# Optimization experiments

Measured on AMD Instinct MI355X. Metric: run time of the kernel, lower is better.

## Reference

```python
import math
import jax, jax.numpy as jnp
from jax import lax
import numpy as np

DIM = 1024
SEED = 2024
N_STEPS = math.ceil(math.log2(DIM) * 0.3) * DIM  # 3072, the KacLayer default


def _make_walk(seed):
    """Seed-derived schedule of Kac random-walk rotations: pairs (i,j), i!=j, and angles."""
    rng = np.random.default_rng(seed)
    ii = rng.integers(0, DIM, N_STEPS).astype(np.int32)
    jj = ((ii + rng.integers(1, DIM, N_STEPS)) % DIM).astype(np.int32)  # guaranteed j != i
    th = rng.uniform(0.0, 2.0 * np.pi, N_STEPS)
    return (jnp.asarray(ii), jnp.asarray(jj),
            jnp.asarray(np.cos(th), dtype=jnp.float32),
            jnp.asarray(np.sin(th), dtype=jnp.float32))

_WALK1 = _make_walk(SEED * 2)      # kac_random_walk_(x, seed*2, n_steps)
_WALK2 = _make_walk(SEED * 2 + 1)  # kac_random_walk_(x, seed*2+1, n_steps)


def _kac_walk(x, walk):
    """Apply N_STEPS sequential 2-coordinate Givens rotations to rows of x [T, DIM]."""
    ii, jj, cs, sn = walk
    def step(x, a):
        i, j, c, s = a
        xi = x[:, i]
        xj = x[:, j]
        x = x.at[:, i].set(c * xi - s * xj)
        x = x.at[:, j].set(s * xi + c * xj)
        return x, None
    x, _ = lax.scan(step, x, (ii, jj, cs, sn))
    return x


def setup_inputs() -> dict:
    key = jax.random.key(0)
    kx, kw, kb, kv = jax.random.split(key, 4)
    x = jax.random.normal(kx, (8, 4096, DIM), dtype=jnp.float32)
    W = jax.random.normal(kw, (DIM, DIM), dtype=jnp.float32) * (1.0 / math.sqrt(DIM))
    b = jax.random.normal(kb, (DIM,), dtype=jnp.float32)
    vec = jax.random.normal(kv, (DIM,), dtype=jnp.float32) * (1.0 / math.sqrt(DIM))
    return {"x": x, "W": W, "b": b, "vec": vec}


def reference(x, W, b, vec):
    # frozen inner layer: y = layer(x)
    y = jnp.einsum("bsd,ed->bse", x, W) + b
    # adapter path on flattened tokens
    x2 = x.reshape(-1, DIM)          # x.view(-1, dim)
    yp = _kac_walk(x2, _WALK1)       # kac_random_walk_(x2, seed*2, n_steps)
    yp = vec * yp                    # elementwise scale by learned vector
    yp = _kac_walk(yp, _WALK2)       # kac_random_walk_(yp, seed*2+1, n_steps)
    return y + yp.reshape(y.shape)
```

## Files before the change

### kernel.cpp

```cpp
#include <hip/hip_runtime.h>


#define NSTEPS 3072
#define NCHUNK 26
#define NRAW (256 * NCHUNK)
#define MAXS 4608
#define MAXLEV 256

typedef __attribute__((ext_vector_type(8))) short short8;
typedef __attribute__((ext_vector_type(4))) float f32x4;

struct U128 { unsigned long long lo, hi; };

__device__ __forceinline__ U128 mul128(U128 a, U128 b) {
  U128 r;
  r.lo = a.lo * b.lo;
  r.hi = __umul64hi(a.lo, b.lo) + a.lo * b.hi + a.hi * b.lo;
  return r;
}
__device__ __forceinline__ U128 add128(U128 a, U128 b) {
  U128 r; r.lo = a.lo + b.lo;
  r.hi = a.hi + b.hi + ((r.lo < a.lo) ? 1ull : 0ull);
  return r;
}
__device__ __forceinline__ U128 pcg_mult() {
  return U128{4865540595714422341ull, 2549297995355413924ull};
}
__device__ __forceinline__ U128 pcg_step(U128 st, U128 inc) {
  return add128(mul128(st, pcg_mult()), inc);
}
__device__ __forceinline__ unsigned long long pcg_out(U128 st) {
  unsigned long long x = st.hi ^ st.lo;
  unsigned int rot = (unsigned int)(st.hi >> 58);
  return (x >> rot) | (x << ((64u - rot) & 63u));
}

__device__ void pcg_seed(unsigned int seedval, U128* st, U128* inc) {
  unsigned int pool[4];
  unsigned int hc = 0x43b0d7e5u;
  auto hashmix = [&hc](unsigned int v) {
    v ^= hc; hc *= 0x931e8875u; v *= hc; v ^= v >> 16; return v;
  };
  auto mixf = [](unsigned int x, unsigned int y) {
    unsigned int r = x * 0xca01f9ddu - y * 0x4973f715u;
    r ^= r >> 16; return r;
  };
  pool[0] = hashmix(seedval);
  pool[1] = hashmix(0u); pool[2] = hashmix(0u); pool[3] = hashmix(0u);
  for (int s = 0; s < 4; ++s)
    for (int d = 0; d < 4; ++d)
      if (s != d) pool[d] = mixf(pool[d], hashmix(pool[s]));
  unsigned int gc = 0x8b51f9ddu;
  unsigned int wv[8];
  for (int k = 0; k < 8; ++k) {
    unsigned int dv = pool[k & 3];
    dv ^= gc; gc *= 0x58f38dedu; dv *= gc; dv ^= dv >> 16;
    wv[k] = dv;
  }
  unsigned long long o0 = (unsigned long long)wv[0] | ((unsigned long long)wv[1] << 32);
  unsigned long long o1 = (unsigned long long)wv[2] | ((unsigned long long)wv[3] << 32);
  unsigned long long o2 = (unsigned long long)wv[4] | ((unsigned long long)wv[5] << 32);
  unsigned long long o3 = (unsigned long long)wv[6] | ((unsigned long long)wv[7] << 32);
  U128 initstate = { o1, o0 };
  U128 initseq   = { o3, o2 };
  U128 icc; icc.lo = (initseq.lo << 1) | 1ull;
  icc.hi = (initseq.hi << 1) | (initseq.lo >> 63);
  *inc = icc;
  U128 s0 = {0ull, 0ull};
  s0 = pcg_step(s0, icc);
  s0 = add128(s0, initstate);
  s0 = pcg_step(s0, icc);
  *st = s0;
}

__device__ U128 pcg_advance(U128 st, U128 inc, unsigned long long delta) {
  U128 am = {1ull, 0ull}, ap = {0ull, 0ull};
  U128 cm = pcg_mult(), cp = inc;
  while (delta) {
    if (delta & 1ull) {
      am = mul128(am, cm);
      ap = add128(mul128(ap, cm), cp);
    }
    cp = mul128(add128(cm, U128{1ull, 0ull}), cp);
    cm = mul128(cm, cm);
    delta >>= 1;
  }
  return add128(mul128(st, am), ap);
}

__device__ __forceinline__ double first_draw(unsigned int seed) {
  U128 st, inc;
  pcg_seed(seed, &st, &inc);
  st = pcg_step(st, inc);
  return (double)(pcg_out(st) >> 11) * (1.0 / 9007199254740992.0);
}

__device__ __forceinline__ unsigned short f32_to_bf16(float f) {
  unsigned int u = __builtin_bit_cast(unsigned int, f);
  unsigned int r = u + 0x7fffu + ((u >> 16) & 1u);
  return (unsigned short)(r >> 16);
}

__global__ __launch_bounds__(256) void gen_sched_kernel(uint4* __restrict__ ps0,
                                                        uint4* __restrict__ ps1,
                                                        int* __restrict__ hdr,
                                                        float* __restrict__ diag) {
  __shared__ unsigned long long raw[NRAW];
  __shared__ unsigned int s_ij[NSTEPS];
  __shared__ unsigned short s_list[2 * NSTEPS];
  __shared__ short s_predA[NSTEPS];
  __shared__ short s_predB[NSTEPS];
  __shared__ unsigned short s_lev[NSTEPS];
  __shared__ int s_cnt[1024];
  __shared__ int s_base[1025];
  __shared__ int s_lcnt[MAXLEV];
  __shared__ int s_lbase[MAXLEV];
  __shared__ int s_rej, s_p64, s_changed, s_maxlev, s_ns;
  const int w = blockIdx.x;
  const int t = threadIdx.x;

  if (w == 0 && t == 0) {
    int m1 = first_draw(42u)    != 0.7739560485559633;
    int m2 = first_draw(0u)     != 0.6369616873214543;
    int m3 = first_draw(12345u) != 0.22733602246716966;
    if (m1 + m2 + m3 >= 2)
      diag[0] = 3.0e8f + (float)(m1 + 2 * m2 + 4 * m3) * 3.0e7f;
  }

  U128 st, inc;
  pcg_seed(4048u + (unsigned int)w, &st, &inc);
  U128 mine = pcg_advance(st, inc, (unsigned long long)t * NCHUNK);
  for (int q = 0; q < NCHUNK; ++q) {
    mine = pcg_step(mine, inc);
    raw[t * NCHUNK + q] = pcg_out(mine);
  }
  if (t == 0) { s_rej = 0; s_maxlev = 1; }
  __syncthreads();

  auto u32at = [&](int m) -> unsigned int {
    unsigned long long v = raw[m >> 1];
    return (m & 1) ? (unsigned int)(v >> 32) : (unsigned int)v;
  };

  for (int k = t; k < NSTEPS; k += 256) {
    unsigned long long m = (unsigned long long)u32at(NSTEPS + k) * 1023ull;
    if ((unsigned int)m < 4u) atomicAdd(&s_rej, 1);
  }
  __syncthreads();

  if (s_rej == 0) {
    for (int k = t; k < NSTEPS; k += 256) {
      unsigned int iv = u32at(k) >> 22;
      unsigned long long m = (unsigned long long)u32at(NSTEPS + k) * 1023ull;
      unsigned int off = 1u + (unsigned int)(m >> 32);
      unsigned int jv = (iv + off) & 1023u;
      s_ij[k] = (iv << 16) | jv;
    }
    if (t == 0) s_p64 = NSTEPS;
  } else if (t == 0) {
    int p = 0;
    for (int k = 0; k < NSTEPS; ++k) s_ij[k] = (u32at(p++) >> 22) << 16;
    for (int k = 0; k < NSTEPS; ++k) {
      unsigned long long m = (unsigned long long)u32at(p++) * 1023ull;
      unsigned int lo = (unsigned int)m;
      if (lo < 1023u) {
        while (lo < 4u) { m = (unsigned long long)u32at(p++) * 1023ull; lo = (unsigned int)m; }
      }
      unsigned int off = 1u + (unsigned int)(m >> 32);
      unsigned int iv = s_ij[k] >> 16;
      s_ij[k] = (iv << 16) | ((iv + off) & 1023u);
    }
    s_p64 = (p + 1) >> 1;
  }
  __syncthreads();

  for (int c = t; c < 1024; c += 256) s_cnt[c] = 0;
  __syncthreads();
  for (int k = t; k < NSTEPS; k += 256) {
    atomicAdd(&s_cnt[s_ij[k] >> 16], 1);
    atomicAdd(&s_cnt[s_ij[k] & 0xffffu], 1);
  }
  __syncthreads();
  if (t < 64) {
    int loc[16], tot = 0;
    #pragma unroll
    for (int q = 0; q < 16; ++q) { loc[q] = s_cnt[t * 16 + q]; tot += loc[q]; }
    int sc = tot;
    for (int off = 1; off < 64; off <<= 1) {
      int v = __shfl_up(sc, off);
      if (t >= off) sc += v;
    }
    int base = sc - tot;
    #pragma unroll
    for (int q = 0; q < 16; ++q) { s_base[t * 16 + q] = base; base += loc[q]; }
  }
  if (t == 0) s_base[1024] = 2 * NSTEPS;
  __syncthreads();

  for (int c = t; c < 1024; c += 256) s_cnt[c] = 0;
  __syncthreads();
  for (int k = t; k < NSTEPS; k += 256) {
    unsigned int iv = s_ij[k] >> 16, jv = s_ij[k] & 0xffffu;
    int p1 = atomicAdd(&s_cnt[iv], 1);
    s_list[s_base[iv] + p1] = (unsigned short)(k << 1);
    int p2 = atomicAdd(&s_cnt[jv], 1);
    s_list[s_base[jv] + p2] = (unsigned short)((k << 1) | 1);
  }
  __syncthreads();
  for (int c = t; c < 1024; c += 256) {
    int b0 = s_base[c], b1 = s_base[c + 1];
    for (int a = b0 + 1; a < b1; ++a) {
      unsigned short v = s_list[a];
      int p = a;
      while (p > b0 && s_list[p - 1] > v) { s_list[p] = s_list[p - 1]; --p; }
      s_list[p] = v;
    }
    short prev = -1;
    for (int a = b0; a < b1; ++a) {
      int e = s_list[a]; int k = e >> 1;
      if (e & 1) s_predB[k] = prev; else s_predA[k] = prev;
      prev = (short)k;
    }
  }
  __syncthreads();

  for (int k = t; k < NSTEPS; k += 256) s_lev[k] = 1;
  __syncthreads();
  for (int it = 0; it < 300; ++it) {
    if (t == 0) s_changed = 0;
    __syncthreads();
    for (int k = t; k < NSTEPS; k += 256) {
      int la = s_predA[k] >= 0 ? (int)s_lev[s_predA[k]] : 0;
      int lb = s_predB[k] >= 0 ? (int)s_lev[s_predB[k]] : 0;
      int nl = 1 + (la > lb ? la : lb);
      if (nl > (int)s_lev[k]) {
        if (nl >= MAXLEV) { nl = MAXLEV - 1; diag[3] = 7.0e8f; }
        s_lev[k] = (unsigned short)nl; s_changed = 1;
      }
    }
    __syncthreads();
    int done = !s_changed;
    __syncthreads();
    if (done) break;
  }

  for (int L = t; L < MAXLEV; L += 256) s_lcnt[L] = 0;
  __syncthreads();
  for (int k = t; k < NSTEPS; k += 256) {
    atomicAdd(&s_lcnt[s_lev[k]], 1);
    atomicMax(&s_maxlev, (int)s_lev[k]);
  }
  __syncthreads();
  if (t == 0) {
    int run = 0;
    for (int L = 1; L <= s_maxlev; ++L) {
      s_lbase[L] = run;
      run += (s_lcnt[L] + 15) & ~15;
    }
    s_ns = run;
    hdr[w] = (run <= MAXS) ? run : MAXS;
    if (run > MAXS) diag[3] = 6.0e8f;
  }
  __syncthreads();
  const int ns = (s_ns <= MAXS) ? s_ns : MAXS;
  uint4* ps = w ? ps1 : ps0;
  uint4 noop;
  noop.x = (17408u << 16) | 17408u;
  noop.y = __float_as_uint(1.0f);
  noop.z = __float_as_uint(0.0f);
  noop.w = 0u;
  for (int s = t; s < ns; s += 256) ps[s] = noop;
  for (int L = t; L < MAXLEV; L += 256) s_lcnt[L] = 0;
  __syncthreads();
  const int base64 = s_p64;
  for (int k = t; k < NSTEPS; k += 256) {
    int lv = s_lev[k];
    int pos = atomicAdd(&s_lcnt[lv], 1);
    int slot = s_lbase[lv] + pos;
    if (slot < MAXS) {
      unsigned long long v = raw[base64 + k];
      double d = (double)(v >> 11) * (1.0 / 9007199254740992.0);
      double ang = d * 6.283185307179586;
      unsigned int ij = s_ij[k];
      unsigned int i17 = (ij >> 16) * 17u, j17 = (ij & 0xffffu) * 17u;
      uint4 ent;
      ent.x = (i17 << 16) | j17;
      ent.y = __float_as_uint((float)cos(ang));
      ent.z = __float_as_uint((float)sin(ang));
      ent.w = 0u;
      ps[slot] = ent;
    }
  }
}

__device__ void walk_groups(const uint4* __restrict__ SG, int ng,
                            float* __restrict__ L, int col, int sub) {
  if (ng <= 0) return;
  uint4 c0 = SG[sub], c1 = SG[sub + 4], c2 = SG[sub + 8], c3 = SG[sub + 12];
  for (int g = 0; g < ng; ++g) {
    const int nb = ((g + 1 < ng) ? (g + 1) : g) << 4;
    uint4 n0 = SG[nb + sub], n1 = SG[nb + sub + 4];
    uint4 n2 = SG[nb + sub + 8], n3 = SG[nb + sub + 12];
    const int i0 = (int)(c0.x >> 16) + col, j0 = (int)(c0.x & 0xffffu) + col;
    const int i1 = (int)(c1.x >> 16) + col, j1 = (int)(c1.x & 0xffffu) + col;
    const int i2 = (int)(c2.x >> 16) + col, j2 = (int)(c2.x & 0xffffu) + col;
    const int i3 = (int)(c3.x >> 16) + col, j3 = (int)(c3.x & 0xffffu) + col;
    float a0 = L[i0], b0 = L[j0], a1 = L[i1], b1 = L[j1];
    float a2 = L[i2], b2 = L[j2], a3 = L[i3], b3 = L[j3];
    const float p0 = __uint_as_float(c0.y), q0 = __uint_as_float(c0.z);
    const float p1 = __uint_as_float(c1.y), q1 = __uint_as_float(c1.z);
    const float p2 = __uint_as_float(c2.y), q2 = __uint_as_float(c2.z);
    const float p3 = __uint_as_float(c3.y), q3 = __uint_as_float(c3.z);
    L[i0] = fmaf(p0, a0, -q0 * b0); L[j0] = fmaf(q0, a0, p0 * b0);
    L[i1] = fmaf(p1, a1, -q1 * b1); L[j1] = fmaf(q1, a1, p1 * b1);
    L[i2] = fmaf(p2, a2, -q2 * b2); L[j2] = fmaf(q2, a2, p2 * b2);
    L[i3] = fmaf(p3, a3, -q3 * b3); L[j3] = fmaf(q3, a3, p3 * b3);
    c0 = n0; c1 = n1; c2 = n2; c3 = n3;
  }
}

__global__ __launch_bounds__(256) void walk_kernel(const uint4* __restrict__ ps0,
                                                   const uint4* __restrict__ ps1,
                                                   const int* __restrict__ hdr,
                                                   const float* __restrict__ W,
                                                   const float* __restrict__ vec,
                                                   unsigned short* __restrict__ Bh,
                                                   float* __restrict__ diag) {
  __shared__ float L[1025 * 17];
  __shared__ uint4 SG[MAXS];
  const int b = blockIdx.x;
  const int t = threadIdx.x;
  const int d0 = b * 16;
  int ns0 = hdr[0]; if (ns0 > MAXS) ns0 = MAXS;
  int ns1 = hdr[1]; if (ns1 > MAXS) ns1 = MAXS;

  for (int idx = t; idx < 1025 * 16; idx += 256) {
    int c = idx >> 4, col = idx & 15;
    L[c * 17 + col] = (c == d0 + col) ? 1.0f : 0.0f;
  }
  for (int s = t; s < ns0; s += 256) SG[s] = ps0[s];
  __syncthreads();
  if (t < 64) walk_groups(SG, ns0 >> 4, L, t & 15, t >> 4);
  __syncthreads();
  {
    bool bad = false;
    if (b == 0 && t < 16) {
      float ss = 0.0f;
      for (int c = 0; c < 1024; ++c) { float v = L[c * 17 + t]; ss += v * v; }
      bad = fabsf(ss - 1.0f) > 2.0e-3f;
    }
    unsigned long long bm = __ballot(bad);
    if (b == 0 && t == 0 && bm) diag[1] = 2.0e7f;
  }
  __syncthreads();
  for (int idx = t; idx < 1024 * 16; idx += 256) {
    int c = idx >> 4, col = idx & 15;
    L[c * 17 + col] *= vec[c];
  }
  for (int s = t; s < ns1; s += 256) SG[s] = ps1[s];
  __syncthreads();
  if (t < 64) walk_groups(SG, ns1 >> 4, L, t & 15, t >> 4);
  __syncthreads();
  const int dl = t & 15;
  const int eb = t >> 4;
  for (int p = 0; p < 64; ++p) {
    int e = eb + p * 16;
    Bh[e * 1024 + d0 + dl] = f32_to_bf16(W[e * 1024 + d0 + dl] + L[e * 17 + dl]);
  }
}

#if __has_builtin(__builtin_amdgcn_global_load_lds)
__device__ __forceinline__ void gload_lds16(const void* g, void* l) {
  __builtin_amdgcn_global_load_lds(
      (const __attribute__((address_space(1))) unsigned int*)g,
      (__attribute__((address_space(3))) unsigned int*)l, 16, 0, 0);
}
#define HAVE_GLDS 1
#else
#define HAVE_GLDS 0
#endif

__global__ __launch_bounds__(256) void gemm_kernel(const float* __restrict__ x,
                                                   const unsigned short* __restrict__ Bhg,
                                                   const float* __restrict__ bvec,
                                                   const float* __restrict__ diag,
                                                   float* __restrict__ out) {
#if HAVE_GLDS
  __shared__ char smem[49152];
  char* Ash = smem;
  char* Bsh = smem + 32768;
  float* Cst = (float*)smem;
  const int t = threadIdx.x;
  const int bidx = blockIdx.x;
  const int xcd = bidx & 7;
  const int kk2 = bidx >> 3;
  const int bm = xcd * 32 + (kk2 >> 3);
  const int bn = kk2 & 7;
  const int m0 = bm * 128, n0 = bn * 128;
  const int l = t & 63, w = t >> 6;
  const int wr = w >> 1, wc = w & 1;
  const int lr = l & 15, lk = l >> 4;
  const int ldsu = w * 1024;

  int arow[8], achb[8];
  #pragma unroll
  for (int p = 0; p < 8; ++p) {
    int idx = p * 256 + t;
    arow[p] = idx >> 4;
    achb[p] = ((idx & 15) ^ (arow[p] & 7)) << 4;
  }
  int brow[4], bchb[4];
  #pragma unroll
  for (int p = 0; p < 4; ++p) {
    int idx = p * 256 + t;
    brow[p] = idx >> 3;
    bchb[p] = ((idx & 7) ^ (brow[p] & 7)) << 4;
  }

  f32x4 acc[4][4] = {};

  for (int kt = 0; kt < 16; ++kt) {
    #pragma unroll
    for (int p = 0; p < 8; ++p)
      gload_lds16((const char*)x + (size_t)(m0 + arow[p]) * 4096 + kt * 256 + achb[p],
                  Ash + p * 4096 + ldsu);
    #pragma unroll
    for (int p = 0; p < 4; ++p)
      gload_lds16((const char*)Bhg + (size_t)(n0 + brow[p]) * 2048 + kt * 128 + bchb[p],
                  Bsh + p * 4096 + ldsu);
    __syncthreads();

    #pragma unroll
    for (int kk = 0; kk < 64; kk += 32) {
      short8 af[4], bf[4];
      #pragma unroll
      for (int m4 = 0; m4 < 4; ++m4) {
        const int r = wr * 64 + m4 * 16 + lr;
        const int c0 = (kk >> 2) + lk * 2;
        const int c0s = c0 ^ (r & 7), c1s = (c0 + 1) ^ (r & 7);
        uint4 lo = *(const uint4*)(Ash + r * 256 + c0s * 16);
        uint4 hi = *(const uint4*)(Ash + r * 256 + c1s * 16);
        uint4 pk;
        pk.x = __byte_perm(lo.x, lo.y, 0x7632);
        pk.y = __byte_perm(lo.z, lo.w, 0x7632);
        pk.z = __byte_perm(hi.x, hi.y, 0x7632);
        pk.w = __byte_perm(hi.z, hi.w, 0x7632);
        af[m4] = __builtin_bit_cast(short8, pk);
      }
      #pragma unroll
      for (int n4 = 0; n4 < 4; ++n4) {
        const int r = wc * 64 + n4 * 16 + lr;
        const int cb = (kk * 2 + lk * 16) ^ ((r & 7) << 4);
        bf[n4] = *(const short8*)(Bsh + r * 128 + cb);
      }
      #pragma unroll
      for (int m4 = 0; m4 < 4; ++m4)
        #pragma unroll
        for (int n4 = 0; n4 < 4; ++n4)
          acc[m4][n4] = __builtin_amdgcn_mfma_f32_16x16x32_bf16(af[m4], bf[n4], acc[m4][n4], 0, 0, 0);
    }
    __syncthreads();
  }

  #pragma unroll
  for (int half = 0; half < 2; ++half) {
    if (wr == half) {
      #pragma unroll
      for (int n4 = 0; n4 < 4; ++n4) {
        const int col = wc * 64 + n4 * 16 + lr;
        const float bias = bvec[n0 + col];
        #pragma unroll
        for (int m4 = 0; m4 < 4; ++m4)
          #pragma unroll
          for (int q = 0; q < 4; ++q)
            Cst[(m4 * 16 + lk * 4 + q) * 132 + col] = acc[m4][n4][q] + bias;
      }
    }
    __syncthreads();
    {
      const int rg = t >> 5;
      const int c4 = (t & 31) * 4;
      #pragma unroll
      for (int rr = 0; rr < 8; ++rr) {
        int r = rg * 8 + rr;
        float4 v = *(const float4*)&Cst[r * 132 + c4];
        *(float4*)&out[(size_t)(m0 + half * 64 + r) * 1024 + (n0 + c4)] = v;
      }
    }
    __syncthreads();
  }

  if (bidx == 0 && t == 0) {
    float dg = diag[0] + diag[1] + diag[3];
    if (dg != 0.0f) out[0] += dg;
  }
#else
  if (blockIdx.x == 0 && threadIdx.x == 0) out[0] = 8.0e8f;
#endif
}

__global__ void signal_kernel(float* out, float val) { out[0] = val; }

extern "C" void kernel_launch(void* const* d_in, const int* in_sizes, int n_in,
                              void* d_out, int out_size, void* d_ws, size_t ws_size,
                              hipStream_t stream) {
  const float* x    = (const float*)d_in[0];
  const float* W    = (const float*)d_in[1];
  const float* bvec = (const float*)d_in[2];
  const float* vec  = (const float*)d_in[3];
  float* out = (float*)d_out;

  const size_t MB = 1024 * 1024;
  const size_t need = 3 * MB;
  if (ws_size < need) {
    signal_kernel<<<1, 1, 0, stream>>>(out, 4.0e8f + (float)(ws_size >> 20) * 1000.0f);
    return;
  }
  float* diag = (float*)d_ws;
  int* hdr = (int*)((char*)d_ws + 256);
  uint4* ps0 = (uint4*)((char*)d_ws + 8192);
  uint4* ps1 = (uint4*)((char*)d_ws + 98304);
  unsigned short* Bh = (unsigned short*)((char*)d_ws + MB);

  hipMemsetAsync(diag, 0, 64, stream);
  gen_sched_kernel<<<2, 256, 0, stream>>>(ps0, ps1, hdr, diag);
  walk_kernel<<<64, 256, 0, stream>>>(ps0, ps1, hdr, W, vec, Bh, diag);
  gemm_kernel<<<2048, 256, 0, stream>>>(x, Bh, bvec, diag, out);
}
```

Measured before the change: 322.8 us.

## Parallelize Kac walk across wavefronts per level and enlarge GEMM tile to 256x128

The schedule generator now exports per-level group boundaries, so the walk kernel can spread the rotation groups of each dependency level over all four wavefronts, with a barrier between levels. Previously only one wavefront walked the whole schedule serially. Separately, the GEMM switches to 512-thread blocks computing 256x128 output tiles, which halves the block count and reuses each B tile across more rows. The costs are many more block barriers in the walk and higher LDS use per GEMM block, which may lower occupancy.

```diff
diff --git a/kernel.cpp b/kernel.cpp
--- a/kernel.cpp
+++ b/kernel.cpp
@@ -104,6 +104,8 @@
 __global__ __launch_bounds__(256) void gen_sched_kernel(uint4* __restrict__ ps0,
                                                         uint4* __restrict__ ps1,
                                                         int* __restrict__ hdr,
+                                                        int* __restrict__ glb0,
+                                                        int* __restrict__ glb1,
                                                         float* __restrict__ diag) {
   __shared__ unsigned long long raw[NRAW];
   __shared__ unsigned int s_ij[NSTEPS];
@@ -118,6 +120,7 @@
   __shared__ int s_rej, s_p64, s_changed, s_maxlev, s_ns;
   const int w = blockIdx.x;
   const int t = threadIdx.x;
+  int* glbw = w ? glb1 : glb0;
 
   if (w == 0 && t == 0) {
     int m1 = first_draw(42u)    != 0.7739560485559633;
@@ -259,10 +262,14 @@
     }
     s_ns = run;
     hdr[w] = (run <= MAXS) ? run : MAXS;
+    hdr[2 + w] = s_maxlev;
     if (run > MAXS) diag[3] = 6.0e8f;
   }
   __syncthreads();
   const int ns = (s_ns <= MAXS) ? s_ns : MAXS;
+  for (int L = 1 + t; L <= s_maxlev; L += 256) glbw[L - 1] = s_lbase[L] >> 4;
+  if (t == 0) glbw[s_maxlev] = ns >> 4;
+
   uint4* ps = w ? ps1 : ps0;
   uint4 noop;
   noop.x = (17408u << 16) | 17408u;
@@ -293,55 +300,59 @@
   }
 }
 
-__device__ void walk_groups(const uint4* __restrict__ SG, int ng,
-                            float* __restrict__ L, int col, int sub) {
-  if (ng <= 0) return;
-  uint4 c0 = SG[sub], c1 = SG[sub + 4], c2 = SG[sub + 8], c3 = SG[sub + 12];
-  for (int g = 0; g < ng; ++g) {
-    const int nb = ((g + 1 < ng) ? (g + 1) : g) << 4;
-    uint4 n0 = SG[nb + sub], n1 = SG[nb + sub + 4];
-    uint4 n2 = SG[nb + sub + 8], n3 = SG[nb + sub + 12];
-    const int i0 = (int)(c0.x >> 16) + col, j0 = (int)(c0.x & 0xffffu) + col;
-    const int i1 = (int)(c1.x >> 16) + col, j1 = (int)(c1.x & 0xffffu) + col;
-    const int i2 = (int)(c2.x >> 16) + col, j2 = (int)(c2.x & 0xffffu) + col;
-    const int i3 = (int)(c3.x >> 16) + col, j3 = (int)(c3.x & 0xffffu) + col;
-    float a0 = L[i0], b0 = L[j0], a1 = L[i1], b1 = L[j1];
-    float a2 = L[i2], b2 = L[j2], a3 = L[i3], b3 = L[j3];
-    const float p0 = __uint_as_float(c0.y), q0 = __uint_as_float(c0.z);
-    const float p1 = __uint_as_float(c1.y), q1 = __uint_as_float(c1.z);
-    const float p2 = __uint_as_float(c2.y), q2 = __uint_as_float(c2.z);
-    const float p3 = __uint_as_float(c3.y), q3 = __uint_as_float(c3.z);
-    L[i0] = fmaf(p0, a0, -q0 * b0); L[j0] = fmaf(q0, a0, p0 * b0);
-    L[i1] = fmaf(p1, a1, -q1 * b1); L[j1] = fmaf(q1, a1, p1 * b1);
-    L[i2] = fmaf(p2, a2, -q2 * b2); L[j2] = fmaf(q2, a2, p2 * b2);
-    L[i3] = fmaf(p3, a3, -q3 * b3); L[j3] = fmaf(q3, a3, p3 * b3);
-    c0 = n0; c1 = n1; c2 = n2; c3 = n3;
-  }
+__device__ __forceinline__ void do_group(const uint4* __restrict__ SG, int g,
+                                         float* __restrict__ L, int col, int sub) {
+  uint4 c0 = SG[g * 16 + sub],     c1 = SG[g * 16 + sub + 4];
+  uint4 c2 = SG[g * 16 + sub + 8], c3 = SG[g * 16 + sub + 12];
+  const int i0 = (int)(c0.x >> 16) + col, j0 = (int)(c0.x & 0xffffu) + col;
+  const int i1 = (int)(c1.x >> 16) + col, j1 = (int)(c1.x & 0xffffu) + col;
+  const int i2 = (int)(c2.x >> 16) + col, j2 = (int)(c2.x & 0xffffu) + col;
+  const int i3 = (int)(c3.x >> 16) + col, j3 = (int)(c3.x & 0xffffu) + col;
+  float a0 = L[i0], b0 = L[j0], a1 = L[i1], b1 = L[j1];
+  float a2 = L[i2], b2 = L[j2], a3 = L[i3], b3 = L[j3];
+  const float p0 = __uint_as_float(c0.y), q0 = __uint_as_float(c0.z);
+  const float p1 = __uint_as_float(c1.y), q1 = __uint_as_float(c1.z);
+  const float p2 = __uint_as_float(c2.y), q2 = __uint_as_float(c2.z);
+  const float p3 = __uint_as_float(c3.y), q3 = __uint_as_float(c3.z);
+  L[i0] = fmaf(p0, a0, -q0 * b0); L[j0] = fmaf(q0, a0, p0 * b0);
+  L[i1] = fmaf(p1, a1, -q1 * b1); L[j1] = fmaf(q1, a1, p1 * b1);
+  L[i2] = fmaf(p2, a2, -q2 * b2); L[j2] = fmaf(q2, a2, p2 * b2);
+  L[i3] = fmaf(p3, a3, -q3 * b3); L[j3] = fmaf(q3, a3, p3 * b3);
 }
 
 __global__ __launch_bounds__(256) void walk_kernel(const uint4* __restrict__ ps0,
                                                    const uint4* __restrict__ ps1,
                                                    const int* __restrict__ hdr,
+                                                   const int* __restrict__ glb0,
+                                                   const int* __restrict__ glb1,
                                                    const float* __restrict__ W,
                                                    const float* __restrict__ vec,
                                                    unsigned short* __restrict__ Bh,
                                                    float* __restrict__ diag) {
   __shared__ float L[1025 * 17];
   __shared__ uint4 SG[MAXS];
+  __shared__ int sGlb[MAXLEV + 1];
   const int b = blockIdx.x;
   const int t = threadIdx.x;
   const int d0 = b * 16;
+  const int wid = t >> 6, lane = t & 63;
+  const int col = lane & 15, sub = lane >> 4;
   int ns0 = hdr[0]; if (ns0 > MAXS) ns0 = MAXS;
   int ns1 = hdr[1]; if (ns1 > MAXS) ns1 = MAXS;
+  const int nlev0 = hdr[2], nlev1 = hdr[3];
 
   for (int idx = t; idx < 1025 * 16; idx += 256) {
-    int c = idx >> 4, col = idx & 15;
-    L[c * 17 + col] = (c == d0 + col) ? 1.0f : 0.0f;
+    int c = idx >> 4, cc = idx & 15;
+    L[c * 17 + cc] = (c == d0 + cc) ? 1.0f : 0.0f;
   }
   for (int s = t; s < ns0; s += 256) SG[s] = ps0[s];
-  __syncthreads();
-  if (t < 64) walk_groups(SG, ns0 >> 4, L, t & 15, t >> 4);
-  __syncthreads();
+  for (int li = t; li <= nlev0 && li <= MAXLEV; li += 256) sGlb[li] = glb0[li];
+  __syncthreads();
+  for (int li = 0; li < nlev0; ++li) {
+    const int g1 = sGlb[li + 1];
+    for (int g = sGlb[li] + wid; g < g1; g += 4) do_group(SG, g, L, col, sub);
+    __syncthreads();
+  }
   {
     bool bad = false;
     if (b == 0 && t < 16) {
@@ -354,13 +365,18 @@
   }
   __syncthreads();
   for (int idx = t; idx < 1024 * 16; idx += 256) {
-    int c = idx >> 4, col = idx & 15;
-    L[c * 17 + col] *= vec[c];
+    int c = idx >> 4, cc = idx & 15;
+    L[c * 17 + cc] *= vec[c];
   }
   for (int s = t; s < ns1; s += 256) SG[s] = ps1[s];
   __syncthreads();
-  if (t < 64) walk_groups(SG, ns1 >> 4, L, t & 15, t >> 4);
-  __syncthreads();
+  for (int li = t; li <= nlev1 && li <= MAXLEV; li += 256) sGlb[li] = glb1[li];
+  __syncthreads();
+  for (int li = 0; li < nlev1; ++li) {
+    const int g1 = sGlb[li + 1];
+    for (int g = sGlb[li] + wid; g < g1; g += 4) do_group(SG, g, L, col, sub);
+    __syncthreads();
+  }
   const int dl = t & 15;
   const int eb = t >> 4;
   for (int p = 0; p < 64; ++p) {
@@ -380,23 +396,23 @@
 #define HAVE_GLDS 0
 #endif
 
-__global__ __launch_bounds__(256) void gemm_kernel(const float* __restrict__ x,
+__global__ __launch_bounds__(512) void gemm_kernel(const float* __restrict__ x,
                                                    const unsigned short* __restrict__ Bhg,
                                                    const float* __restrict__ bvec,
                                                    const float* __restrict__ diag,
                                                    float* __restrict__ out) {
 #if HAVE_GLDS
-  __shared__ char smem[49152];
+  __shared__ char smem[81920];
   char* Ash = smem;
-  char* Bsh = smem + 32768;
+  char* Bsh = smem + 65536;
   float* Cst = (float*)smem;
   const int t = threadIdx.x;
   const int bidx = blockIdx.x;
   const int xcd = bidx & 7;
   const int kk2 = bidx >> 3;
-  const int bm = xcd * 32 + (kk2 >> 3);
+  const int bm = xcd * 16 + (kk2 >> 3);
   const int bn = kk2 & 7;
-  const int m0 = bm * 128, n0 = bn * 128;
+  const int m0 = bm * 256, n0 = bn * 128;
   const int l = t & 63, w = t >> 6;
   const int wr = w >> 1, wc = w & 1;
   const int lr = l & 15, lk = l >> 4;
@@ -405,14 +421,14 @@
   int arow[8], achb[8];
   #pragma unroll
   for (int p = 0; p < 8; ++p) {
-    int idx = p * 256 + t;
+    int idx = p * 512 + t;
     arow[p] = idx >> 4;
     achb[p] = ((idx & 15) ^ (arow[p] & 7)) << 4;
   }
-  int brow[4], bchb[4];
+  int brow[2], bchb[2];
   #pragma unroll
-  for (int p = 0; p < 4; ++p) {
-    int idx = p * 256 + t;
+  for (int p = 0; p < 2; ++p) {
+    int idx = p * 512 + t;
     brow[p] = idx >> 3;
     bchb[p] = ((idx & 7) ^ (brow[p] & 7)) << 4;
   }
@@ -423,11 +439,11 @@
     #pragma unroll
     for (int p = 0; p < 8; ++p)
       gload_lds16((const char*)x + (size_t)(m0 + arow[p]) * 4096 + kt * 256 + achb[p],
-                  Ash + p * 4096 + ldsu);
+                  Ash + p * 8192 + ldsu);
     #pragma unroll
-    for (int p = 0; p < 4; ++p)
+    for (int p = 0; p < 2; ++p)
       gload_lds16((const char*)Bhg + (size_t)(n0 + brow[p]) * 2048 + kt * 128 + bchb[p],
-                  Bsh + p * 4096 + ldsu);
+                  Bsh + p * 8192 + ldsu);
     __syncthreads();
 
     #pragma unroll
@@ -463,28 +479,28 @@
   }
 
   #pragma unroll
-  for (int half = 0; half < 2; ++half) {
-    if (wr == half) {
+  for (int quarter = 0; quarter < 4; ++quarter) {
+    if (wr == quarter) {
       #pragma unroll
       for (int n4 = 0; n4 < 4; ++n4) {
-        const int col = wc * 64 + n4 * 16 + lr;
-        const float bias = bvec[n0 + col];
+        const int cc = wc * 64 + n4 * 16 + lr;
+        const float bias = bvec[n0 + cc];
         #pragma unroll
         for (int m4 = 0; m4 < 4; ++m4)
           #pragma unroll
           for (int q = 0; q < 4; ++q)
-            Cst[(m4 * 16 + lk * 4 + q) * 132 + col] = acc[m4][n4][q] + bias;
+            Cst[(m4 * 16 + lk * 4 + q) * 132 + cc] = acc[m4][n4][q] + bias;
       }
     }
     __syncthreads();
     {
-      const int rg = t >> 5;
       const int c4 = (t & 31) * 4;
+      const int rbase = t >> 5;
       #pragma unroll
-      for (int rr = 0; rr < 8; ++rr) {
-        int r = rg * 8 + rr;
+      for (int rr = 0; rr < 4; ++rr) {
+        int r = rbase + rr * 16;
         float4 v = *(const float4*)&Cst[r * 132 + c4];
-        *(float4*)&out[(size_t)(m0 + half * 64 + r) * 1024 + (n0 + c4)] = v;
+        *(float4*)&out[(size_t)(m0 + quarter * 64 + r) * 1024 + (n0 + c4)] = v;
       }
     }
     __syncthreads();
@@ -518,12 +534,14 @@
   }
   float* diag = (float*)d_ws;
   int* hdr = (int*)((char*)d_ws + 256);
+  int* glb0 = (int*)((char*)d_ws + 1024);
+  int* glb1 = (int*)((char*)d_ws + 2560);
   uint4* ps0 = (uint4*)((char*)d_ws + 8192);
   uint4* ps1 = (uint4*)((char*)d_ws + 98304);
   unsigned short* Bh = (unsigned short*)((char*)d_ws + MB);
 
   hipMemsetAsync(diag, 0, 64, stream);
-  gen_sched_kernel<<<2, 256, 0, stream>>>(ps0, ps1, hdr, diag);
-  walk_kernel<<<64, 256, 0, stream>>>(ps0, ps1, hdr, W, vec, Bh, diag);
-  gemm_kernel<<<2048, 256, 0, stream>>>(x, Bh, bvec, diag, out);
-}
+  gen_sched_kernel<<<2, 256, 0, stream>>>(ps0, ps1, hdr, glb0, glb1, diag);
+  walk_kernel<<<64, 256, 0, stream>>>(ps0, ps1, hdr, glb0, glb1, W, vec, Bh, diag);
+  gemm_kernel<<<1024, 512, 0, stream>>>(x, Bh, bvec, diag, out);
+}
```

After: 329.9 us. +2.2%, slower.

## Parallelize Kac walk across levels with four wavefronts and more blocks

Applied to the files above, without the earlier changes.

The walk kernel previously ran the rotation schedule with a single wavefront per block over 16 columns, in fixed groups of 16. It now processes 4 columns per block across 256 blocks and splits each dependency level's groups among all four wavefronts, with a block barrier between levels. The schedule generator emits level boundaries and stores raw indices, since the new LDS stride is 5. This adds many __syncthreads and assumes rotations within a level are independent.

```diff
diff --git a/kernel.cpp b/kernel.cpp
--- a/kernel.cpp
+++ b/kernel.cpp
@@ -104,6 +104,8 @@
 __global__ __launch_bounds__(256) void gen_sched_kernel(uint4* __restrict__ ps0,
                                                         uint4* __restrict__ ps1,
                                                         int* __restrict__ hdr,
+                                                        int* __restrict__ glb0,
+                                                        int* __restrict__ glb1,
                                                         float* __restrict__ diag) {
   __shared__ unsigned long long raw[NRAW];
   __shared__ unsigned int s_ij[NSTEPS];
@@ -118,6 +120,7 @@
   __shared__ int s_rej, s_p64, s_changed, s_maxlev, s_ns;
   const int w = blockIdx.x;
   const int t = threadIdx.x;
+  int* glbw = w ? glb1 : glb0;
 
   if (w == 0 && t == 0) {
     int m1 = first_draw(42u)    != 0.7739560485559633;
@@ -259,13 +262,17 @@
     }
     s_ns = run;
     hdr[w] = (run <= MAXS) ? run : MAXS;
+    hdr[2 + w] = s_maxlev;
     if (run > MAXS) diag[3] = 6.0e8f;
   }
   __syncthreads();
   const int ns = (s_ns <= MAXS) ? s_ns : MAXS;
+  for (int L = 1 + t; L <= s_maxlev; L += 256) glbw[L - 1] = s_lbase[L] >> 4;
+  if (t == 0) glbw[s_maxlev] = ns >> 4;
+
   uint4* ps = w ? ps1 : ps0;
   uint4 noop;
-  noop.x = (17408u << 16) | 17408u;
+  noop.x = (1024u << 16) | 1024u;
   noop.y = __float_as_uint(1.0f);
   noop.z = __float_as_uint(0.0f);
   noop.w = 0u;
@@ -281,10 +288,8 @@
       unsigned long long v = raw[base64 + k];
       double d = (double)(v >> 11) * (1.0 / 9007199254740992.0);
       double ang = d * 6.283185307179586;
-      unsigned int ij = s_ij[k];
-      unsigned int i17 = (ij >> 16) * 17u, j17 = (ij & 0xffffu) * 17u;
       uint4 ent;
-      ent.x = (i17 << 16) | j17;
+      ent.x = s_ij[k];
       ent.y = __float_as_uint((float)cos(ang));
       ent.z = __float_as_uint((float)sin(ang));
       ent.w = 0u;
@@ -293,79 +298,78 @@
   }
 }
 
-__device__ void walk_groups(const uint4* __restrict__ SG, int ng,
-                            float* __restrict__ L, int col, int sub) {
-  if (ng <= 0) return;
-  uint4 c0 = SG[sub], c1 = SG[sub + 4], c2 = SG[sub + 8], c3 = SG[sub + 12];
-  for (int g = 0; g < ng; ++g) {
-    const int nb = ((g + 1 < ng) ? (g + 1) : g) << 4;
-    uint4 n0 = SG[nb + sub], n1 = SG[nb + sub + 4];
-    uint4 n2 = SG[nb + sub + 8], n3 = SG[nb + sub + 12];
-    const int i0 = (int)(c0.x >> 16) + col, j0 = (int)(c0.x & 0xffffu) + col;
-    const int i1 = (int)(c1.x >> 16) + col, j1 = (int)(c1.x & 0xffffu) + col;
-    const int i2 = (int)(c2.x >> 16) + col, j2 = (int)(c2.x & 0xffffu) + col;
-    const int i3 = (int)(c3.x >> 16) + col, j3 = (int)(c3.x & 0xffffu) + col;
-    float a0 = L[i0], b0 = L[j0], a1 = L[i1], b1 = L[j1];
-    float a2 = L[i2], b2 = L[j2], a3 = L[i3], b3 = L[j3];
-    const float p0 = __uint_as_float(c0.y), q0 = __uint_as_float(c0.z);
-    const float p1 = __uint_as_float(c1.y), q1 = __uint_as_float(c1.z);
-    const float p2 = __uint_as_float(c2.y), q2 = __uint_as_float(c2.z);
-    const float p3 = __uint_as_float(c3.y), q3 = __uint_as_float(c3.z);
-    L[i0] = fmaf(p0, a0, -q0 * b0); L[j0] = fmaf(q0, a0, p0 * b0);
-    L[i1] = fmaf(p1, a1, -q1 * b1); L[j1] = fmaf(q1, a1, p1 * b1);
-    L[i2] = fmaf(p2, a2, -q2 * b2); L[j2] = fmaf(q2, a2, p2 * b2);
-    L[i3] = fmaf(p3, a3, -q3 * b3); L[j3] = fmaf(q3, a3, p3 * b3);
-    c0 = n0; c1 = n1; c2 = n2; c3 = n3;
-  }
+__device__ __forceinline__ void do_group(const uint4* __restrict__ SG, int g,
+                                         float* __restrict__ L, int col, int slot) {
+  uint4 e = SG[g * 16 + slot];
+  const int i = (int)(e.x >> 16) * 5 + col, j = (int)(e.x & 0xffffu) * 5 + col;
+  const float c = __uint_as_float(e.y), s = __uint_as_float(e.z);
+  float xi = L[i], xj = L[j];
+  L[i] = fmaf(c, xi, -s * xj);
+  L[j] = fmaf(s, xi, c * xj);
 }
 
 __global__ __launch_bounds__(256) void walk_kernel(const uint4* __restrict__ ps0,
                                                    const uint4* __restrict__ ps1,
                                                    const int* __restrict__ hdr,
+                                                   const int* __restrict__ glb0,
+                                                   const int* __restrict__ glb1,
                                                    const float* __restrict__ W,
                                                    const float* __restrict__ vec,
                                                    unsigned short* __restrict__ Bh,
                                                    float* __restrict__ diag) {
-  __shared__ float L[1025 * 17];
+  __shared__ float L[1025 * 5];
   __shared__ uint4 SG[MAXS];
+  __shared__ int sGlb[MAXLEV + 1];
   const int b = blockIdx.x;
   const int t = threadIdx.x;
-  const int d0 = b * 16;
+  const int d0 = b * 4;
+  const int wid = t >> 6, lane = t & 63;
+  const int col = lane & 3, slot = lane >> 2;
   int ns0 = hdr[0]; if (ns0 > MAXS) ns0 = MAXS;
   int ns1 = hdr[1]; if (ns1 > MAXS) ns1 = MAXS;
-
-  for (int idx = t; idx < 1025 * 16; idx += 256) {
-    int c = idx >> 4, col = idx & 15;
-    L[c * 17 + col] = (c == d0 + col) ? 1.0f : 0.0f;
+  const int nlev0 = hdr[2], nlev1 = hdr[3];
+
+  for (int idx = t; idx < 1025 * 4; idx += 256) {
+    int c = idx >> 2, cc = idx & 3;
+    L[c * 5 + cc] = (c == d0 + cc) ? 1.0f : 0.0f;
   }
   for (int s = t; s < ns0; s += 256) SG[s] = ps0[s];
-  __syncthreads();
-  if (t < 64) walk_groups(SG, ns0 >> 4, L, t & 15, t >> 4);
-  __syncthreads();
+  for (int li = t; li <= nlev0 && li <= MAXLEV; li += 256) sGlb[li] = glb0[li];
+  __syncthreads();
+  for (int li = 0; li < nlev0; ++li) {
+    const int g1 = sGlb[li + 1];
+    for (int g = sGlb[li] + wid; g < g1; g += 4) do_group(SG, g, L, col, slot);
+    __syncthreads();
+  }
   {
     bool bad = false;
-    if (b == 0 && t < 16) {
+    if (b == 0 && t < 4) {
       float ss = 0.0f;
-      for (int c = 0; c < 1024; ++c) { float v = L[c * 17 + t]; ss += v * v; }
+      for (int c = 0; c < 1024; ++c) { float v = L[c * 5 + t]; ss += v * v; }
       bad = fabsf(ss - 1.0f) > 2.0e-3f;
     }
     unsigned long long bm = __ballot(bad);
     if (b == 0 && t == 0 && bm) diag[1] = 2.0e7f;
   }
   __syncthreads();
-  for (int idx = t; idx < 1024 * 16; idx += 256) {
-    int c = idx >> 4, col = idx & 15;
-    L[c * 17 + col] *= vec[c];
+  for (int idx = t; idx < 1024 * 4; idx += 256) {
+    int c = idx >> 2, cc = idx & 3;
+    L[c * 5 + cc] *= vec[c];
   }
   for (int s = t; s < ns1; s += 256) SG[s] = ps1[s];
   __syncthreads();
-  if (t < 64) walk_groups(SG, ns1 >> 4, L, t & 15, t >> 4);
-  __syncthreads();
-  const int dl = t & 15;
-  const int eb = t >> 4;
-  for (int p = 0; p < 64; ++p) {
-    int e = eb + p * 16;
-    Bh[e * 1024 + d0 + dl] = f32_to_bf16(W[e * 1024 + d0 + dl] + L[e * 17 + dl]);
+  for (int li = t; li <= nlev1 && li <= MAXLEV; li += 256) sGlb[li] = glb1[li];
+  __syncthreads();
+  for (int li = 0; li < nlev1; ++li) {
+    const int g1 = sGlb[li + 1];
+    for (int g = sGlb[li] + wid; g < g1; g += 4) do_group(SG, g, L, col, slot);
+    __syncthreads();
+  }
+  const int dl = t & 3;
+  const int eb = t >> 2;
+  for (int p = 0; p < 16; ++p) {
+    int e = eb + p * 64;
+    Bh[e * 1024 + d0 + dl] = f32_to_bf16(W[e * 1024 + d0 + dl] + L[e * 5 + dl]);
   }
 }
 
@@ -518,12 +522,14 @@
   }
   float* diag = (float*)d_ws;
   int* hdr = (int*)((char*)d_ws + 256);
+  int* glb0 = (int*)((char*)d_ws + 1024);
+  int* glb1 = (int*)((char*)d_ws + 2560);
   uint4* ps0 = (uint4*)((char*)d_ws + 8192);
   uint4* ps1 = (uint4*)((char*)d_ws + 98304);
   unsigned short* Bh = (unsigned short*)((char*)d_ws + MB);
 
   hipMemsetAsync(diag, 0, 64, stream);
-  gen_sched_kernel<<<2, 256, 0, stream>>>(ps0, ps1, hdr, diag);
-  walk_kernel<<<64, 256, 0, stream>>>(ps0, ps1, hdr, W, vec, Bh, diag);
+  gen_sched_kernel<<<2, 256, 0, stream>>>(ps0, ps1, hdr, glb0, glb1, diag);
+  walk_kernel<<<256, 256, 0, stream>>>(ps0, ps1, hdr, glb0, glb1, W, vec, Bh, diag);
   gemm_kernel<<<2048, 256, 0, stream>>>(x, Bh, bvec, diag, out);
 }
```

Result: faster. 269.7 us, median of 2 (-16.4%).
